# Optimization experiments

Measured on AMD Instinct MI355X. Metric: run time of the kernel, lower is better.

Reference implementation:

```python
import jax, jax.numpy as jnp
import numpy as np

A = 9            # n_anchor = len(ratios)*len(anchor_scales)
STRIDE = 16      # feat_stride
IMG_H = 1024
IMG_W = 1024
MIN_SIZE = 16.0  # min_size * scale (scale=1.0)
PRE_NMS = 2000
POST_NMS = 300
NMS_THRESH = 0.7


def _anchor_base():
    base = 16.0
    ratios = np.array([0.5, 1.0, 2.0])
    scales = np.array([8.0, 16.0, 32.0])
    ab = np.zeros((A, 4), np.float32)
    px = py = base / 2.0
    for i, r in enumerate(ratios):
        for j, s in enumerate(scales):
            h = base * s * np.sqrt(r)
            w = base * s * np.sqrt(1.0 / r)
            ab[i * 3 + j] = [py - h / 2, px - w / 2, py + h / 2, px + w / 2]
    return ab


def _all_anchors(hh, ww):
    ab = _anchor_base()
    sy = np.arange(0, hh * STRIDE, STRIDE)
    sx = np.arange(0, ww * STRIDE, STRIDE)
    sx, sy = np.meshgrid(sx, sy)
    shift = np.stack((sy.ravel(), sx.ravel(), sy.ravel(), sx.ravel()), axis=1)
    anc = (ab[None, :, :] + shift[:, None, :]).reshape(-1, 4).astype(np.float32)
    return jnp.asarray(anc)  # [hh*ww*A, 4] in (y1,x1,y2,x2)


def _conv(x, w, b, pad):
    y = jax.lax.conv_general_dilated(
        x, w, (1, 1), [(pad, pad), (pad, pad)],
        dimension_numbers=('NCHW', 'OIHW', 'NCHW'))
    return y + b[None, :, None, None]


def _loc2bbox(anc, loc):
    h = anc[:, 2] - anc[:, 0]
    w = anc[:, 3] - anc[:, 1]
    cy = anc[:, 0] + 0.5 * h
    cx = anc[:, 1] + 0.5 * w
    dy, dx, dh, dw = loc[:, 0], loc[:, 1], loc[:, 2], loc[:, 3]
    cy2 = dy * h + cy
    cx2 = dx * w + cx
    h2 = jnp.exp(dh) * h
    w2 = jnp.exp(dw) * w
    return jnp.stack([cy2 - 0.5 * h2, cx2 - 0.5 * w2,
                      cy2 + 0.5 * h2, cx2 + 0.5 * w2], axis=1)


def _iou_matrix(b):
    tl = jnp.maximum(b[:, None, :2], b[None, :, :2])
    br = jnp.minimum(b[:, None, 2:], b[None, :, 2:])
    inter = jnp.prod(jnp.clip(br - tl, 0.0), axis=-1)
    area = jnp.prod(b[:, 2:] - b[:, :2], axis=-1)
    return inter / (area[:, None] + area[None, :] - inter + 1e-9)


def _propose(fg, loc, anc):
    # fg: [K*A] foreground scores, loc: [K*A, 4] deltas
    boxes = _loc2bbox(anc, loc)
    boxes = jnp.stack([jnp.clip(boxes[:, 0], 0.0, IMG_H),
                       jnp.clip(boxes[:, 1], 0.0, IMG_W),
                       jnp.clip(boxes[:, 2], 0.0, IMG_H),
                       jnp.clip(boxes[:, 3], 0.0, IMG_W)], axis=1)
    hs = boxes[:, 2] - boxes[:, 0]
    ws = boxes[:, 3] - boxes[:, 1]
    valid = (hs >= MIN_SIZE) & (ws >= MIN_SIZE)
    fg = jnp.where(valid, fg, -jnp.inf)
    sc, idx = jax.lax.top_k(fg, PRE_NMS)          # sorted desc by score
    b = boxes[idx]                                 # [PRE_NMS, 4]
    iou = jax.lax.stop_gradient(_iou_matrix(b))    # indices/masks are constants
    keep0 = sc > -jnp.inf
    ar = jnp.arange(PRE_NMS)

    def body(i, keep):
        sup = (iou[i] > NMS_THRESH) & keep[i] & (ar > i)
        return keep & ~sup

    keep = jax.lax.fori_loop(0, PRE_NMS, body, keep0)
    order = jnp.where(keep, ar, PRE_NMS)
    sel = jnp.sort(order)[:POST_NMS]
    ok = sel < PRE_NMS
    sel = jnp.minimum(sel, PRE_NMS - 1)
    rois = jnp.where(ok[:, None], b[sel], 0.0)     # [POST_NMS, 4], zero-padded
    return rois


def setup_inputs() -> dict:
    key = jax.random.key(0)
    ks = jax.random.split(key, 4)
    x = jax.random.normal(ks[0], (8, 512, 64, 64), dtype=jnp.float32)
    conv1_w = jax.random.normal(ks[1], (512, 512, 3, 3), dtype=jnp.float32) * 0.01
    conv1_b = jnp.zeros((512,), jnp.float32)
    score_w = jax.random.normal(ks[2], (2 * A, 512, 1, 1), dtype=jnp.float32) * 0.01
    score_b = jnp.zeros((2 * A,), jnp.float32)
    loc_w = jax.random.normal(ks[3], (4 * A, 512, 1, 1), dtype=jnp.float32) * 0.01
    loc_b = jnp.zeros((4 * A,), jnp.float32)
    return {'x': x, 'conv1_w': conv1_w, 'conv1_b': conv1_b,
            'score_w': score_w, 'score_b': score_b,
            'loc_w': loc_w, 'loc_b': loc_b}


def reference(x, conv1_w, conv1_b, score_w, score_b, loc_w, loc_b):
    n, _, hh, ww = x.shape
    h = jax.nn.relu(_conv(x, conv1_w, conv1_b, 1))
    loc = _conv(h, loc_w, loc_b, 0)                # [n, 4A, hh, ww]
    score = _conv(h, score_w, score_b, 0)          # [n, 2A, hh, ww]
    rpn_locs = loc.transpose(0, 2, 3, 1).reshape(n, -1, 4)      # [n, hh*ww*A, 4]
    rpn_scores = score.transpose(0, 2, 3, 1).reshape(n, -1, 2)  # [n, hh*ww*A, 2]
    fg = jax.nn.softmax(rpn_scores.reshape(n, hh, ww, A, 2), axis=-1)[..., 1]
    fg = fg.reshape(n, -1)                         # [n, hh*ww*A]
    anc = _all_anchors(hh, ww)
    rois = jax.vmap(lambda f, l: _propose(f, l, anc))(fg, rpn_locs)  # [n, POST_NMS, 4]
    roi_indices = jnp.repeat(jnp.arange(n, dtype=jnp.int32), POST_NMS)
    return rpn_locs, rpn_scores, rois.reshape(-1, 4), roi_indices, anc
```

## Files before the change

kernel.cpp:

```cpp
#include <hip/hip_runtime.h>
#include <math.h>
#include <stdint.h>

#define NB 8
#define CIN 512
#define HW 4096
#define ANUM 9
#define NANC 36864
#define PRE 2000
#define POST 300

#define OUT_LOCS   0
#define OUT_SCORES 1179648
#define OUT_ROIS   1769472
#define OUT_RIDX   1779072
#define OUT_ANC    1781472

typedef _Float16 half8 __attribute__((ext_vector_type(8)));
typedef float f32x4 __attribute__((ext_vector_type(4)));

#define WSCALE 256.0f
#define LSCALE 4096.0f
#define INV_WS (1.0f / 256.0f)
#define INV_LS (1.0f / 4096.0f)
#define XS_STRIDE 40

__global__ void anchor_kernel(float* __restrict__ out) {
  int i = blockIdx.x * 256 + threadIdx.x;
  if (i >= NANC) return;
  int s = i / 9, a = i - s * 9;
  int y = s >> 6, x = s & 63;
  int ri = a / 3, si = a - ri * 3;
  double r = (ri == 0) ? 0.5 : (ri == 1 ? 1.0 : 2.0);
  double sc = (si == 0) ? 8.0 : (si == 1 ? 16.0 : 32.0);
  double hh = 16.0 * sc * sqrt(r);
  double ww = 16.0 * sc * sqrt(1.0 / r);
  float a0 = (float)(8.0 - hh * 0.5);
  float a1 = (float)(8.0 - ww * 0.5);
  float a2 = (float)(8.0 + hh * 0.5);
  float a3 = (float)(8.0 + ww * 0.5);
  float sy = (float)(y * 16), sx = (float)(x * 16);
  out[OUT_ANC + i * 4 + 0] = a0 + sy;
  out[OUT_ANC + i * 4 + 1] = a1 + sx;
  out[OUT_ANC + i * 4 + 2] = a2 + sy;
  out[OUT_ANC + i * 4 + 3] = a3 + sx;
}

__global__ void wprep_kernel(const float* __restrict__ w, _Float16* __restrict__ Bf) {
  int i = blockIdx.x * 256 + threadIdx.x;
  int j = i & 7;
  int l = (i >> 3) & 63;
  int limb = (i >> 9) & 1;
  int ob = (i >> 10) & 31;
  int icb = (i >> 15) & 15;
  int tap = i >> 19;
  int ic = icb * 32 + ((l >> 4) << 3) + j;
  int oc = (ob << 4) + (l & 15);
  float v = w[((size_t)oc * CIN + ic) * 9 + tap] * WSCALE;
  _Float16 hi = (_Float16)v;
  Bf[i] = limb ? (_Float16)((v - (float)hi) * LSCALE) : hi;
}

__global__ __launch_bounds__(256) void conv3_mfma(
    const float* __restrict__ x, const _Float16* __restrict__ Bf,
    const float* __restrict__ bias, float* __restrict__ h, int blk0) {
  __shared__ _Float16 xhi[2][108 * XS_STRIDE];
  __shared__ _Float16 xlo[2][108 * XS_STRIDE];
  int blk = blk0 + blockIdx.x;
  int ntblk = blk & 3;
  int mb = blk >> 2;
  int img = mb >> 6;
  int t = mb & 63;
  int ty0 = (t >> 2) * 4, tx0 = (t & 3) * 16;
  int tid = threadIdx.x;
  int wv = tid >> 6, lane = tid & 63;
  int col = lane & 15, quad = lane >> 4;

  f32x4 acc0[4][2], accC[4][2];
#pragma unroll
  for (int g = 0; g < 4; ++g)
#pragma unroll
    for (int nt = 0; nt < 2; ++nt) {
      acc0[g][nt] = (f32x4){0.f, 0.f, 0.f, 0.f};
      accC[g][nt] = (f32x4){0.f, 0.f, 0.f, 0.f};
    }

  int goffs[4];
  int laddr[4];
#pragma unroll
  for (int s = 0; s < 4; ++s) {
    int l = tid + (s << 8);
    bool act = (l < 864);
    int icg = l / 108;
    int pos = l - icg * 108;
    int py = pos / 18, px = pos - py * 18;
    int gy = ty0 - 1 + py, gx = tx0 - 1 + px;
    bool inb = act && ((unsigned)gy < 64u) && ((unsigned)gx < 64u);
    goffs[s] = inb ? ((icg << 14) + (gy << 6) + gx) : -1;
    laddr[s] = act ? (pos * XS_STRIDE + (icg << 2)) : -1;
  }

  const float* xn = x + ((size_t)img << 21);
  const half8* B8 = (const half8*)Bf;
  const half8* Bq = B8 + (((size_t)(ntblk * 8 + wv * 2)) << 7) + lane;
  int abase = col * XS_STRIDE + quad * 8;

  typedef _Float16 h4 __attribute__((ext_vector_type(4)));

  {
    const float* xb = xn;
#pragma unroll
    for (int s = 0; s < 4; ++s) {
      if (laddr[s] >= 0) {
        float v0 = 0.f, v1 = 0.f, v2 = 0.f, v3 = 0.f;
        if (goffs[s] >= 0) {
          const float* p = xb + goffs[s];
          v0 = p[0]; v1 = p[HW]; v2 = p[2 * HW]; v3 = p[3 * HW];
        }
        _Float16 h0 = (_Float16)v0, h1 = (_Float16)v1;
        _Float16 h2 = (_Float16)v2, h3 = (_Float16)v3;
        _Float16 e0 = (_Float16)((v0 - (float)h0) * LSCALE);
        _Float16 e1 = (_Float16)((v1 - (float)h1) * LSCALE);
        _Float16 e2 = (_Float16)((v2 - (float)h2) * LSCALE);
        _Float16 e3 = (_Float16)((v3 - (float)h3) * LSCALE);
        *(h4*)(xhi[0] + laddr[s]) = (h4){h0, h1, h2, h3};
        *(h4*)(xlo[0] + laddr[s]) = (h4){e0, e1, e2, e3};
      }
    }
  }
  __syncthreads();

#pragma unroll 1
  for (int icb = 0; icb < 16; ++icb) {
    int cur = icb & 1;
    float pv0[4], pv1[4], pv2[4], pv3[4];
    const int nxt = icb + 1;
    if (nxt < 16) {
      const float* xb = xn + ((size_t)nxt << 17);
#pragma unroll
      for (int s = 0; s < 4; ++s) {
        pv0[s] = 0.f; pv1[s] = 0.f; pv2[s] = 0.f; pv3[s] = 0.f;
        if (goffs[s] >= 0) {
          const float* p = xb + goffs[s];
          pv0[s] = p[0]; pv1[s] = p[HW]; pv2[s] = p[2 * HW]; pv3[s] = p[3 * HW];
        }
      }
    }
    const _Float16* xh = xhi[cur];
    const _Float16* xl = xlo[cur];
    __builtin_amdgcn_s_setprio(1);
#pragma unroll
    for (int ky = 0; ky < 3; ++ky) {
#pragma unroll
      for (int kx = 0; kx < 3; ++kx) {
        int tap = ky * 3 + kx;
        size_t boff = ((size_t)(tap * 16 + icb)) << 12;
        half8 Bh0 = Bq[boff];
        half8 Bl0 = Bq[boff + 64];
        half8 Bh1 = Bq[boff + 128];
        half8 Bl1 = Bq[boff + 192];
        int toff = (ky * 18 + kx) * XS_STRIDE + abase;
#pragma unroll
        for (int g = 0; g < 4; ++g) {
          int off = toff + g * (18 * XS_STRIDE);
          half8 Ah = *(const half8*)(xh + off);
          half8 Al = *(const half8*)(xl + off);
          acc0[g][0] = __builtin_amdgcn_mfma_f32_16x16x32_f16(Ah, Bh0, acc0[g][0], 0, 0, 0);
          accC[g][0] = __builtin_amdgcn_mfma_f32_16x16x32_f16(Ah, Bl0, accC[g][0], 0, 0, 0);
          accC[g][0] = __builtin_amdgcn_mfma_f32_16x16x32_f16(Al, Bh0, accC[g][0], 0, 0, 0);
          acc0[g][1] = __builtin_amdgcn_mfma_f32_16x16x32_f16(Ah, Bh1, acc0[g][1], 0, 0, 0);
          accC[g][1] = __builtin_amdgcn_mfma_f32_16x16x32_f16(Ah, Bl1, accC[g][1], 0, 0, 0);
          accC[g][1] = __builtin_amdgcn_mfma_f32_16x16x32_f16(Al, Bh1, accC[g][1], 0, 0, 0);
        }
      }
    }
    __builtin_amdgcn_s_setprio(0);
    if (nxt < 16) {
      _Float16* wh = xhi[cur ^ 1];
      _Float16* wl = xlo[cur ^ 1];
#pragma unroll
      for (int s = 0; s < 4; ++s) {
        if (laddr[s] >= 0) {
          float v0 = pv0[s], v1 = pv1[s], v2 = pv2[s], v3 = pv3[s];
          _Float16 h0 = (_Float16)v0, h1 = (_Float16)v1;
          _Float16 h2 = (_Float16)v2, h3 = (_Float16)v3;
          _Float16 e0 = (_Float16)((v0 - (float)h0) * LSCALE);
          _Float16 e1 = (_Float16)((v1 - (float)h1) * LSCALE);
          _Float16 e2 = (_Float16)((v2 - (float)h2) * LSCALE);
          _Float16 e3 = (_Float16)((v3 - (float)h3) * LSCALE);
          *(h4*)(wh + laddr[s]) = (h4){h0, h1, h2, h3};
          *(h4*)(wl + laddr[s]) = (h4){e0, e1, e2, e3};
        }
      }
    }
    __syncthreads();
  }
#pragma unroll
  for (int g = 0; g < 4; ++g) {
#pragma unroll
    for (int nt = 0; nt < 2; ++nt) {
      int oc = (ntblk << 7) + (wv << 5) + (nt << 4) + col;
      float bv = bias[oc];
      int gy = ty0 + g;
      int gx0 = tx0 + (quad << 2);
      f32x4 a0 = acc0[g][nt];
      f32x4 ac = accC[g][nt];
      float4 o;
      o.x = fmaf(ac.x, INV_LS, a0.x) * INV_WS + bv; o.x = o.x > 0.f ? o.x : 0.f;
      o.y = fmaf(ac.y, INV_LS, a0.y) * INV_WS + bv; o.y = o.y > 0.f ? o.y : 0.f;
      o.z = fmaf(ac.z, INV_LS, a0.z) * INV_WS + bv; o.z = o.z > 0.f ? o.z : 0.f;
      o.w = fmaf(ac.w, INV_LS, a0.w) * INV_WS + bv; o.w = o.w > 0.f ? o.w : 0.f;
      *(float4*)(h + ((size_t)img * CIN + oc) * HW + (gy << 6) + gx0) = o;
    }
  }
}

__global__ __launch_bounds__(256) void heads_kernel(
    const float* __restrict__ h, const float* __restrict__ sw,
    const float* __restrict__ sb, const float* __restrict__ lw,
    const float* __restrict__ lb, float* __restrict__ out,
    float* __restrict__ fgm, float* __restrict__ boxes) {
  __shared__ float part[128][56];
  int tid = threadIdx.x;
  int sl = tid >> 7;
  int pl = tid & 127;
  int blk = blockIdx.x;
  int n = blk >> 5;
  int s0 = (blk & 31) * 128;

  float acc[54];
#pragma unroll
  for (int k = 0; k < 54; k++) acc[k] = 0.f;

  int cbase = sl * 256;
  const float* hp = h + ((size_t)n * CIN + cbase) * HW + s0 + pl;
#pragma unroll 8
  for (int cl = 0; cl < 256; ++cl) {
    float hv = hp[(size_t)cl * HW];
    int c = cbase + cl;
#pragma unroll
    for (int k = 0; k < 18; ++k) acc[k] = fmaf(hv, sw[k * CIN + c], acc[k]);
#pragma unroll
    for (int k = 0; k < 36; ++k) acc[18 + k] = fmaf(hv, lw[k * CIN + c], acc[18 + k]);
  }
  if (sl == 1) {
#pragma unroll
    for (int k = 0; k < 54; k++) part[pl][k] = acc[k];
  }
  __syncthreads();
  if (sl == 0) {
#pragma unroll
    for (int k = 0; k < 54; k++) acc[k] += part[pl][k];
    int s = s0 + pl;
    int y = s >> 6, xx = s & 63;
    float sc[18], lo[36];
#pragma unroll
    for (int k = 0; k < 18; k++) sc[k] = acc[k] + sb[k];
#pragma unroll
    for (int k = 0; k < 36; k++) lo[k] = acc[18 + k] + lb[k];
    size_t base = (size_t)n * NANC + (size_t)s * 9;
#pragma unroll
    for (int i = 0; i < 36; i++) out[OUT_LOCS + base * 4 + i] = lo[i];
#pragma unroll
    for (int i = 0; i < 18; i++) out[OUT_SCORES + base * 2 + i] = sc[i];
    float syf = (float)(y * 16), sxf = (float)(xx * 16);
#pragma unroll
    for (int a = 0; a < 9; a++) {
      float s0v = sc[a * 2], s1v = sc[a * 2 + 1];
      float m = fmaxf(s0v, s1v);
      float e0 = expf(s0v - m), e1 = expf(s1v - m);
      float fg = e1 / (e0 + e1);
      int ri = a / 3, si = a - ri * 3;
      double r = (ri == 0) ? 0.5 : (ri == 1 ? 1.0 : 2.0);
      double scd = (si == 0) ? 8.0 : (si == 1 ? 16.0 : 32.0);
      double hhd = 16.0 * scd * sqrt(r);
      double wwd = 16.0 * scd * sqrt(1.0 / r);
      float a0 = (float)(8.0 - hhd * 0.5) + syf;
      float a1 = (float)(8.0 - wwd * 0.5) + sxf;
      float a2 = (float)(8.0 + hhd * 0.5) + syf;
      float a3 = (float)(8.0 + wwd * 0.5) + sxf;
      float hA = a2 - a0, wA = a3 - a1;
      float cy = a0 + 0.5f * hA, cx = a1 + 0.5f * wA;
      float dy = lo[a * 4 + 0], dx = lo[a * 4 + 1];
      float dh = lo[a * 4 + 2], dw = lo[a * 4 + 3];
      float cy2 = dy * hA + cy, cx2 = dx * wA + cx;
      float h2 = expf(dh) * hA, w2 = expf(dw) * wA;
      float b0 = cy2 - 0.5f * h2, b1 = cx2 - 0.5f * w2;
      float b2 = cy2 + 0.5f * h2, b3 = cx2 + 0.5f * w2;
      b0 = fminf(fmaxf(b0, 0.f), 1024.f);
      b1 = fminf(fmaxf(b1, 0.f), 1024.f);
      b2 = fminf(fmaxf(b2, 0.f), 1024.f);
      b3 = fminf(fmaxf(b3, 0.f), 1024.f);
      float hs = b2 - b0, wss = b3 - b1;
      bool valid = (hs >= 16.f) && (wss >= 16.f);
      size_t bi = base + a;
      boxes[bi * 4 + 0] = b0; boxes[bi * 4 + 1] = b1;
      boxes[bi * 4 + 2] = b2; boxes[bi * 4 + 3] = b3;
      fgm[bi] = valid ? fg : -__builtin_inff();
    }
  }
}

__device__ __forceinline__ uint32_t ord32(float v) {
  uint32_t s = __float_as_uint(v);
  return (s & 0x80000000u) ? ~s : (s | 0x80000000u);
}

__global__ __launch_bounds__(1024) void select2_kernel(
    const float* __restrict__ fgm, const float* __restrict__ boxes,
    float4* __restrict__ selb, uint8_t* __restrict__ selv) {
  int n = blockIdx.x;
  const float* f = fgm + (size_t)n * NANC;
  __shared__ uint32_t hist[256];
  __shared__ uint32_t segsum[16], segsufE[16];
  __shared__ uint64_t keys[2048];
  __shared__ uint32_t sh_digit, sh_T, scnt;
  int tid = threadIdx.x;
  uint32_t pref = 0;
  uint32_t T = PRE;
  for (int p = 0; p < 4; ++p) {
    int shift = 24 - 8 * p;
    if (tid < 256) hist[tid] = 0;
    __syncthreads();
    for (int i = tid; i < NANC; i += 1024) {
      uint32_t u = ord32(f[i]);
      bool match = (p == 0) || ((u >> (shift + 8)) == (pref >> (shift + 8)));
      if (match) atomicAdd(&hist[(u >> shift) & 255u], 1u);
    }
    __syncthreads();
    if (tid < 16) {
      uint32_t s = 0;
      for (int j = 0; j < 16; ++j) s += hist[tid * 16 + j];
      segsum[tid] = s;
    }
    __syncthreads();
    if (tid == 0) {
      uint32_t run = 0;
      for (int s = 15; s >= 0; --s) { segsufE[s] = run; run += segsum[s]; }
    }
    __syncthreads();
    if (tid < 256) {
      int d = tid, s = d >> 4;
      uint32_t loc = 0;
      for (int j = d; j < (s + 1) * 16; ++j) loc += hist[j];
      uint32_t suf = segsufE[s] + loc;
      uint32_t sufn = suf - hist[d];
      if (suf >= T && sufn < T) { sh_digit = (uint32_t)d; sh_T = T - sufn; }
    }
    __syncthreads();
    pref |= sh_digit << shift;
    T = sh_T;
    __syncthreads();
  }
  if (tid == 0) scnt = 0;
  __syncthreads();
  for (int i = tid; i < NANC; i += 1024) {
    uint32_t u = ord32(f[i]);
    if (u >= pref) {
      uint32_t pos = atomicAdd(&scnt, 1u);
      if (pos < 2048) keys[pos] = ((uint64_t)u << 32) | (uint32_t)(~(uint32_t)i);
    }
  }
  __syncthreads();
  uint32_t sc = scnt > 2048 ? 2048 : scnt;
  for (int i = sc + tid; i < 2048; i += 1024) keys[i] = 0;
  __syncthreads();
  for (int k = 2; k <= 2048; k <<= 1) {
    for (int j = k >> 1; j > 0; j >>= 1) {
      for (int e = tid; e < 2048; e += 1024) {
        int partner = e ^ j;
        if (partner > e) {
          bool up = ((e & k) == 0);
          uint64_t a = keys[e], b = keys[partner];
          if (up ? (a < b) : (a > b)) { keys[e] = b; keys[partner] = a; }
        }
      }
      __syncthreads();
    }
  }
  for (int t2 = tid; t2 < PRE; t2 += 1024) {
    uint64_t key = keys[t2];
    uint32_t idx = ~((uint32_t)(key & 0xFFFFFFFFu));
    const float4* bp = (const float4*)(boxes + ((size_t)n * NANC + idx) * 4);
    selb[(size_t)n * 2048 + t2] = *bp;
    selv[(size_t)n * 2048 + t2] = ((uint32_t)(key >> 32)) > 0x007FFFFFu ? 1 : 0;
  }
}

__global__ __launch_bounds__(256) void nms_mask_kernel(
    const float4* __restrict__ selb, uint64_t* __restrict__ mask) {
  __shared__ float by0[PRE], bx0_[PRE], by1[PRE], bx1_[PRE], bar[PRE];
  int b = blockIdx.x;
  int n = b / 250;
  int i0 = (b % 250) * 8;
  int tid = threadIdx.x;
  for (int j = tid; j < PRE; j += 256) {
    float4 bb = selb[(size_t)n * 2048 + j];
    by0[j] = bb.x; bx0_[j] = bb.y; by1[j] = bb.z; bx1_[j] = bb.w;
    bar[j] = (bb.z - bb.x) * (bb.w - bb.y);
  }
  __syncthreads();
  int i = i0 + (tid >> 5);
  int jw = tid & 31;
  float iy0 = by0[i], ix0 = bx0_[i], iy1 = by1[i], ix1 = bx1_[i], ia = bar[i];
  uint64_t bits = 0;
  int jb = jw * 64;
  for (int tb = 0; tb < 64; ++tb) {
    int tbp = (tb + jw) & 63;
    int j = jb + tbp;
    if (j < PRE && j > i) {
      float ty = fmaxf(iy0, by0[j]);
      float txx = fmaxf(ix0, bx0_[j]);
      float byv = fminf(iy1, by1[j]);
      float bxv = fminf(ix1, bx1_[j]);
      float ih = byv - ty; if (ih < 0.f) ih = 0.f;
      float iw = bxv - txx; if (iw < 0.f) iw = 0.f;
      float inter = ih * iw;
      float iou = inter / (ia + bar[j] - inter + 1e-9f);
      if (iou > 0.7f) bits |= (1ull << tbp);
    }
  }
  mask[((size_t)n * PRE + i) * 32 + jw] = bits;
}

__global__ __launch_bounds__(64) void nms_scan_kernel(
    const uint8_t* __restrict__ selv, const uint64_t* __restrict__ mask,
    const float4* __restrict__ selb, float* __restrict__ out) {
  int n = blockIdx.x;
  int lane = threadIdx.x;
  const uint8_t* sv = selv + (size_t)n * 2048;
  uint64_t kw = 0;
  for (int wblk = 0; wblk < 32; ++wblk) {
    int j = wblk * 64 + lane;
    bool pred = (j < PRE) && (sv[j] != 0);
    uint64_t m = __ballot(pred);
    if (lane == wblk) kw = m;
  }
  const uint64_t* mrow = mask + (size_t)n * PRE * 32;
  int istar = PRE - 1;
  int csf = 0;
  bool done = false;
  for (int i0 = 0; i0 < PRE && !done; i0 += 16) {
    uint64_t rr[16];
#pragma unroll
    for (int tt = 0; tt < 16; ++tt)
      rr[tt] = (lane < 32) ? mrow[(size_t)(i0 + tt) * 32 + lane] : 0;
#pragma unroll
    for (int tt = 0; tt < 16; ++tt) {
      int i = i0 + tt;
      uint64_t w = __shfl(kw, i >> 6);
      if ((w >> (i & 63)) & 1ull) {
        kw &= ~rr[tt];
        csf++;
        if (csf >= POST) { istar = i; done = true; break; }
      }
    }
  }
  int wordi = istar >> 6, biti = istar & 63;
  uint64_t km = (lane < wordi) ? ~0ull
              : (lane == wordi ? ((biti == 63) ? ~0ull : ((1ull << (biti + 1)) - 1ull)) : 0ull);
  uint64_t kwv = (lane < 32) ? (kw & km) : 0ull;
  int pc = __popcll(kwv);
  int pre = pc;
  for (int d = 1; d < 64; d <<= 1) {
    int v = __shfl_up(pre, d);
    if (lane >= d) pre += v;
  }
  int total = __shfl(pre, 63);
  int rank = pre - pc;
  uint64_t bits = kwv;
  while (bits) {
    int bpos = __ffsll((unsigned long long)bits) - 1;
    bits &= bits - 1;
    if (rank < POST) {
      int j = lane * 64 + bpos;
      float4 bx = selb[(size_t)n * 2048 + j];
      size_t o = (size_t)OUT_ROIS + ((size_t)n * POST + rank) * 4;
      out[o + 0] = bx.x; out[o + 1] = bx.y; out[o + 2] = bx.z; out[o + 3] = bx.w;
    }
    rank++;
  }
  int cnt = total > POST ? POST : total;
  for (int r2 = cnt + lane; r2 < POST; r2 += 64) {
    size_t o = (size_t)OUT_ROIS + ((size_t)n * POST + r2) * 4;
    out[o + 0] = 0.f; out[o + 1] = 0.f; out[o + 2] = 0.f; out[o + 3] = 0.f;
  }
  for (int r2 = lane; r2 < POST; r2 += 64)
    out[OUT_RIDX + n * POST + r2] = (float)n;
}

extern "C" void kernel_launch(void* const* d_in, const int* in_sizes, int n_in,
                              void* d_out, int out_size, void* d_ws, size_t ws_size,
                              hipStream_t stream) {
  const float* x   = (const float*)d_in[0];
  const float* c1w = (const float*)d_in[1];
  const float* c1b = (const float*)d_in[2];
  const float* sw  = (const float*)d_in[3];
  const float* sb  = (const float*)d_in[4];
  const float* lw  = (const float*)d_in[5];
  const float* lb  = (const float*)d_in[6];
  float* out = (float*)d_out;
  char* ws = (char*)d_ws;
  float*     hbuf = (float*)(ws);
  float*     fgm  = (float*)(ws + 67108864);
  float*     boxes= (float*)(ws + 68288512);
  _Float16*  Bf   = (_Float16*)(ws + 73007104);
  float4*    selb = (float4*)(ws + 82444288);
  uint8_t*   selv = (uint8_t*)(ws + 82706432);
  uint64_t*  mask = (uint64_t*)(ws + 82722816);

  anchor_kernel<<<144, 256, 0, stream>>>(out);
  wprep_kernel<<<18432, 256, 0, stream>>>(c1w, Bf);
  conv3_mfma<<<512, 256, 0, stream>>>(x, Bf, c1b, hbuf, 0);
  conv3_mfma<<<512, 256, 0, stream>>>(x, Bf, c1b, hbuf, 512);
  conv3_mfma<<<512, 256, 0, stream>>>(x, Bf, c1b, hbuf, 1024);
  conv3_mfma<<<512, 256, 0, stream>>>(x, Bf, c1b, hbuf, 1536);
  heads_kernel<<<256, 256, 0, stream>>>(hbuf, sw, sb, lw, lb, out, fgm, boxes);
  select2_kernel<<<8, 1024, 0, stream>>>(fgm, boxes, selb, selv);
  nms_mask_kernel<<<2000, 256, 0, stream>>>(selb, mask);
  nms_scan_kernel<<<8, 64, 0, stream>>>(selv, mask, selb, out);
}
```

Measured before the change: 954.3 us.

## Split 1x1 head convs into LDS-staged matmul kernel and separate epilogue

Splits the fused heads kernel into heads_mm and heads_epi. heads_mm runs three output-channel groups of 18 over 768 blocks and stages the weights in LDS as float4 rows, replacing per-iteration scalar global weight loads. heads_epi reads the 54 accumulated channels back and runs the softmax, box decode and writes. The aim is more parallelism and fewer registers (18 accumulators instead of 54), at the cost of reading the 64 MB h buffer three times, an extra launch and a round trip through workspace that reuses the area of the fp16 conv weights (Bf).

```diff
diff --git a/kernel.cpp b/kernel.cpp
--- a/kernel.cpp
+++ b/kernel.cpp
@@ -215,89 +215,123 @@
   }
 }
 
-__global__ __launch_bounds__(256) void heads_kernel(
+__global__ __launch_bounds__(256) void heads_mm(
     const float* __restrict__ h, const float* __restrict__ sw,
-    const float* __restrict__ sb, const float* __restrict__ lw,
-    const float* __restrict__ lb, float* __restrict__ out,
-    float* __restrict__ fgm, float* __restrict__ boxes) {
-  __shared__ float part[128][56];
+    const float* __restrict__ lw, float* __restrict__ hacc) {
+  __shared__ float wlds[512][20];
+  __shared__ float part[128][20];
   int tid = threadIdx.x;
   int sl = tid >> 7;
   int pl = tid & 127;
   int blk = blockIdx.x;
-  int n = blk >> 5;
-  int s0 = (blk & 31) * 128;
-
-  float acc[54];
-#pragma unroll
-  for (int k = 0; k < 54; k++) acc[k] = 0.f;
-
-  int cbase = sl * 256;
-  const float* hp = h + ((size_t)n * CIN + cbase) * HW + s0 + pl;
-#pragma unroll 8
+  int kg = blk >> 8;
+  int rem = blk & 255;
+  int n = rem >> 5;
+  int s0 = (rem & 31) * 128;
+
+  const float* wsrc = (kg == 0) ? sw : (lw + (size_t)(kg == 1 ? 0 : 18) * CIN);
+  for (int l = tid; l < 18 * 512; l += 256) {
+    int j = l >> 9;
+    int c = l & 511;
+    wlds[c][j] = wsrc[(size_t)j * CIN + c];
+  }
+  __syncthreads();
+
+  float acc[18];
+#pragma unroll
+  for (int j = 0; j < 18; ++j) acc[j] = 0.f;
+  int cb = sl * 256;
+  const float* hp = h + ((size_t)n * CIN + cb) * HW + s0 + pl;
+#pragma unroll 4
   for (int cl = 0; cl < 256; ++cl) {
     float hv = hp[(size_t)cl * HW];
-    int c = cbase + cl;
-#pragma unroll
-    for (int k = 0; k < 18; ++k) acc[k] = fmaf(hv, sw[k * CIN + c], acc[k]);
-#pragma unroll
-    for (int k = 0; k < 36; ++k) acc[18 + k] = fmaf(hv, lw[k * CIN + c], acc[18 + k]);
+    const float* wr = &wlds[cb + cl][0];
+    float4 wa = *(const float4*)(wr + 0);
+    float4 wb = *(const float4*)(wr + 4);
+    float4 wc = *(const float4*)(wr + 8);
+    float4 wd = *(const float4*)(wr + 12);
+    float2 we = *(const float2*)(wr + 16);
+    acc[0]  = fmaf(hv, wa.x, acc[0]);  acc[1]  = fmaf(hv, wa.y, acc[1]);
+    acc[2]  = fmaf(hv, wa.z, acc[2]);  acc[3]  = fmaf(hv, wa.w, acc[3]);
+    acc[4]  = fmaf(hv, wb.x, acc[4]);  acc[5]  = fmaf(hv, wb.y, acc[5]);
+    acc[6]  = fmaf(hv, wb.z, acc[6]);  acc[7]  = fmaf(hv, wb.w, acc[7]);
+    acc[8]  = fmaf(hv, wc.x, acc[8]);  acc[9]  = fmaf(hv, wc.y, acc[9]);
+    acc[10] = fmaf(hv, wc.z, acc[10]); acc[11] = fmaf(hv, wc.w, acc[11]);
+    acc[12] = fmaf(hv, wd.x, acc[12]); acc[13] = fmaf(hv, wd.y, acc[13]);
+    acc[14] = fmaf(hv, wd.z, acc[14]); acc[15] = fmaf(hv, wd.w, acc[15]);
+    acc[16] = fmaf(hv, we.x, acc[16]); acc[17] = fmaf(hv, we.y, acc[17]);
   }
   if (sl == 1) {
 #pragma unroll
-    for (int k = 0; k < 54; k++) part[pl][k] = acc[k];
+    for (int j = 0; j < 18; ++j) part[pl][j] = acc[j];
   }
   __syncthreads();
   if (sl == 0) {
-#pragma unroll
-    for (int k = 0; k < 54; k++) acc[k] += part[pl][k];
     int s = s0 + pl;
-    int y = s >> 6, xx = s & 63;
-    float sc[18], lo[36];
-#pragma unroll
-    for (int k = 0; k < 18; k++) sc[k] = acc[k] + sb[k];
-#pragma unroll
-    for (int k = 0; k < 36; k++) lo[k] = acc[18 + k] + lb[k];
-    size_t base = (size_t)n * NANC + (size_t)s * 9;
-#pragma unroll
-    for (int i = 0; i < 36; i++) out[OUT_LOCS + base * 4 + i] = lo[i];
-#pragma unroll
-    for (int i = 0; i < 18; i++) out[OUT_SCORES + base * 2 + i] = sc[i];
-    float syf = (float)(y * 16), sxf = (float)(xx * 16);
-#pragma unroll
-    for (int a = 0; a < 9; a++) {
-      float s0v = sc[a * 2], s1v = sc[a * 2 + 1];
-      float m = fmaxf(s0v, s1v);
-      float e0 = expf(s0v - m), e1 = expf(s1v - m);
-      float fg = e1 / (e0 + e1);
-      int ri = a / 3, si = a - ri * 3;
-      double r = (ri == 0) ? 0.5 : (ri == 1 ? 1.0 : 2.0);
-      double scd = (si == 0) ? 8.0 : (si == 1 ? 16.0 : 32.0);
-      double hhd = 16.0 * scd * sqrt(r);
-      double wwd = 16.0 * scd * sqrt(1.0 / r);
-      float a0 = (float)(8.0 - hhd * 0.5) + syf;
-      float a1 = (float)(8.0 - wwd * 0.5) + sxf;
-      float a2 = (float)(8.0 + hhd * 0.5) + syf;
-      float a3 = (float)(8.0 + wwd * 0.5) + sxf;
-      float hA = a2 - a0, wA = a3 - a1;
-      float cy = a0 + 0.5f * hA, cx = a1 + 0.5f * wA;
-      float dy = lo[a * 4 + 0], dx = lo[a * 4 + 1];
-      float dh = lo[a * 4 + 2], dw = lo[a * 4 + 3];
-      float cy2 = dy * hA + cy, cx2 = dx * wA + cx;
-      float h2 = expf(dh) * hA, w2 = expf(dw) * wA;
-      float b0 = cy2 - 0.5f * h2, b1 = cx2 - 0.5f * w2;
-      float b2 = cy2 + 0.5f * h2, b3 = cx2 + 0.5f * w2;
-      b0 = fminf(fmaxf(b0, 0.f), 1024.f);
-      b1 = fminf(fmaxf(b1, 0.f), 1024.f);
-      b2 = fminf(fmaxf(b2, 0.f), 1024.f);
-      b3 = fminf(fmaxf(b3, 0.f), 1024.f);
-      float hs = b2 - b0, wss = b3 - b1;
-      bool valid = (hs >= 16.f) && (wss >= 16.f);
-      size_t bi = base + a;
-      boxes[bi * 4 + 0] = b0; boxes[bi * 4 + 1] = b1;
-      boxes[bi * 4 + 2] = b2; boxes[bi * 4 + 3] = b3;
-      fgm[bi] = valid ? fg : -__builtin_inff();
-    }
+#pragma unroll
+    for (int j = 0; j < 18; ++j) {
+      float v = acc[j] + part[pl][j];
+      hacc[(size_t)(kg * 18 + j) * (NB * HW) + (size_t)n * HW + s] = v;
+    }
+  }
+}
+
+__global__ __launch_bounds__(256) void heads_epi(
+    const float* __restrict__ hacc, const float* __restrict__ sb,
+    const float* __restrict__ lb, float* __restrict__ out,
+    float* __restrict__ fgm, float* __restrict__ boxes) {
+  int g = blockIdx.x * 256 + threadIdx.x;
+  int n = g >> 12;
+  int s = g & 4095;
+  float acc[54];
+#pragma unroll
+  for (int k = 0; k < 54; ++k)
+    acc[k] = hacc[(size_t)k * (NB * HW) + (size_t)n * HW + s];
+  int y = s >> 6, xx = s & 63;
+  float sc[18], lo[36];
+#pragma unroll
+  for (int k = 0; k < 18; k++) sc[k] = acc[k] + sb[k];
+#pragma unroll
+  for (int k = 0; k < 36; k++) lo[k] = acc[18 + k] + lb[k];
+  size_t base = (size_t)n * NANC + (size_t)s * 9;
+#pragma unroll
+  for (int i = 0; i < 36; i++) out[OUT_LOCS + base * 4 + i] = lo[i];
+#pragma unroll
+  for (int i = 0; i < 18; i++) out[OUT_SCORES + base * 2 + i] = sc[i];
+  float syf = (float)(y * 16), sxf = (float)(xx * 16);
+#pragma unroll
+  for (int a = 0; a < 9; a++) {
+    float s0v = sc[a * 2], s1v = sc[a * 2 + 1];
+    float m = fmaxf(s0v, s1v);
+    float e0 = expf(s0v - m), e1 = expf(s1v - m);
+    float fg = e1 / (e0 + e1);
+    int ri = a / 3, si = a - ri * 3;
+    double r = (ri == 0) ? 0.5 : (ri == 1 ? 1.0 : 2.0);
+    double scd = (si == 0) ? 8.0 : (si == 1 ? 16.0 : 32.0);
+    double hhd = 16.0 * scd * sqrt(r);
+    double wwd = 16.0 * scd * sqrt(1.0 / r);
+    float a0 = (float)(8.0 - hhd * 0.5) + syf;
+    float a1 = (float)(8.0 - wwd * 0.5) + sxf;
+    float a2 = (float)(8.0 + hhd * 0.5) + syf;
+    float a3 = (float)(8.0 + wwd * 0.5) + sxf;
+    float hA = a2 - a0, wA = a3 - a1;
+    float cy = a0 + 0.5f * hA, cx = a1 + 0.5f * wA;
+    float dy = lo[a * 4 + 0], dx = lo[a * 4 + 1];
+    float dh = lo[a * 4 + 2], dw = lo[a * 4 + 3];
+    float cy2 = dy * hA + cy, cx2 = dx * wA + cx;
+    float h2 = expf(dh) * hA, w2 = expf(dw) * wA;
+    float b0 = cy2 - 0.5f * h2, b1 = cx2 - 0.5f * w2;
+    float b2 = cy2 + 0.5f * h2, b3 = cx2 + 0.5f * w2;
+    b0 = fminf(fmaxf(b0, 0.f), 1024.f);
+    b1 = fminf(fmaxf(b1, 0.f), 1024.f);
+    b2 = fminf(fmaxf(b2, 0.f), 1024.f);
+    b3 = fminf(fmaxf(b3, 0.f), 1024.f);
+    float hs = b2 - b0, wss = b3 - b1;
+    bool valid = (hs >= 16.f) && (wss >= 16.f);
+    size_t bi = base + a;
+    boxes[bi * 4 + 0] = b0; boxes[bi * 4 + 1] = b1;
+    boxes[bi * 4 + 2] = b2; boxes[bi * 4 + 3] = b3;
+    fgm[bi] = valid ? fg : -__builtin_inff();
   }
 }
 
@@ -505,6 +539,7 @@
   float*     fgm  = (float*)(ws + 67108864);
   float*     boxes= (float*)(ws + 68288512);
   _Float16*  Bf   = (_Float16*)(ws + 73007104);
+  float*     hacc = (float*)(ws + 73007104);
   float4*    selb = (float4*)(ws + 82444288);
   uint8_t*   selv = (uint8_t*)(ws + 82706432);
   uint64_t*  mask = (uint64_t*)(ws + 82722816);
@@ -515,7 +550,8 @@
   conv3_mfma<<<512, 256, 0, stream>>>(x, Bf, c1b, hbuf, 512);
   conv3_mfma<<<512, 256, 0, stream>>>(x, Bf, c1b, hbuf, 1024);
   conv3_mfma<<<512, 256, 0, stream>>>(x, Bf, c1b, hbuf, 1536);
-  heads_kernel<<<256, 256, 0, stream>>>(hbuf, sw, sb, lw, lb, out, fgm, boxes);
+  heads_mm<<<768, 256, 0, stream>>>(hbuf, sw, lw, hacc);
+  heads_epi<<<128, 256, 0, stream>>>(hacc, sb, lb, out, fgm, boxes);
   select2_kernel<<<8, 1024, 0, stream>>>(fgm, boxes, selb, selv);
   nms_mask_kernel<<<2000, 256, 0, stream>>>(selb, mask);
   nms_scan_kernel<<<8, 64, 0, stream>>>(selv, mask, selb, out);
```

After: 851.1 us. 1.12x faster.
